# Kernel optimization log

Measured on AMD Instinct MI355X. Metric: run time of the kernel, lower is better.

The kernel has to match this reference:

```python
import jax, jax.numpy as jnp
import numpy as np

HIDDEN = 2048
NUM_HEADS = 16
NUM_KV_HEADS = 4
HEAD_DIM = HIDDEN // NUM_HEADS  # 128
GROUPS = NUM_HEADS // NUM_KV_HEADS  # 4
ROPE_DIMS = 32
QK_GAIN = 6.0
B, T = 2, 2048


def _rope_cos_sin(T, dtype):
    pos = jnp.arange(T, dtype=jnp.float32)
    inv_freq = 1.0 / (10000.0 ** (jnp.arange(0, ROPE_DIMS, 2, dtype=jnp.float32) / ROPE_DIMS))
    freqs = jnp.outer(pos, inv_freq)                  # [T, ROPE/2]
    freqs = jnp.concatenate([freqs, freqs], axis=-1)  # [T, ROPE]
    return jnp.cos(freqs).astype(dtype), jnp.sin(freqs).astype(dtype)


def _apply_rope(t, cos_f, sin_f):
    # t: [B, H, T, head_dim]; rope on first ROPE_DIMS, pass-through on the rest
    t_rt, t_pass = t[..., :ROPE_DIMS], t[..., ROPE_DIMS:]
    h1, h2 = jnp.split(t_rt, 2, axis=-1)
    rot = jnp.concatenate([-h2, h1], axis=-1)
    return jnp.concatenate([t_rt * cos_f + rot * sin_f, t_pass], axis=-1)


def setup_inputs() -> dict:
    key = jax.random.key(0)
    ks = jax.random.split(key, 5)
    s = 0.02
    return {
        "x": jax.random.normal(ks[0], (B, T, HIDDEN), jnp.float32),
        "Wq": jax.random.normal(ks[1], (HIDDEN, HIDDEN), jnp.float32) * s,
        "Wk": jax.random.normal(ks[2], (HIDDEN, NUM_KV_HEADS * HEAD_DIM), jnp.float32) * s,
        "Wv": jax.random.normal(ks[3], (HIDDEN, NUM_KV_HEADS * HEAD_DIM), jnp.float32) * s,
        "Wo": jax.random.normal(ks[4], (HIDDEN, HIDDEN), jnp.float32) * s,
    }


def reference(x, Wq, Wk, Wv, Wo):
    Bx, Tx, C = x.shape
    q = (x @ Wq).reshape(Bx, Tx, NUM_HEADS, HEAD_DIM).transpose(0, 2, 1, 3)      # [B,H,T,d]
    k = (x @ Wk).reshape(Bx, Tx, NUM_KV_HEADS, HEAD_DIM).transpose(0, 2, 1, 3)   # [B,KV,T,d]
    v = (x @ Wv).reshape(Bx, Tx, NUM_KV_HEADS, HEAD_DIM).transpose(0, 2, 1, 3)   # [B,KV,T,d]

    cos_f, sin_f = _rope_cos_sin(Tx, q.dtype)  # [T, ROPE]
    q = _apply_rope(q, cos_f, sin_f)
    k = _apply_rope(k, cos_f, sin_f)

    # GQA: group query heads per kv head instead of repeat_interleave-ing K/V
    qg = q.reshape(Bx, NUM_KV_HEADS, GROUPS, Tx, HEAD_DIM)
    scale = QK_GAIN / jnp.sqrt(jnp.asarray(HEAD_DIM, q.dtype))
    scores = jnp.einsum('bkgqd,bkld->bkgql', qg * scale, k)  # [B,KV,G,T,T]
    causal = jnp.tril(jnp.ones((Tx, Tx), dtype=bool))
    scores = jnp.where(causal, scores, jnp.asarray(-jnp.inf, scores.dtype))
    probs = jax.nn.softmax(scores, axis=-1)
    out = jnp.einsum('bkgql,bkld->bkgqd', probs, v)          # [B,KV,G,T,d]
    out = out.reshape(Bx, NUM_HEADS, Tx, HEAD_DIM).transpose(0, 2, 1, 3).reshape(Bx, Tx, C)
    return out @ Wo
```

## Files before the change

### kernel.cpp

```cpp
#include <hip/hip_runtime.h>
#include <hip/hip_bf16.h>
#include <cstdint>
#include <cstddef>

typedef unsigned short u16;
typedef short s16x8 __attribute__((ext_vector_type(8)));
typedef float f32x4 __attribute__((ext_vector_type(4)));
typedef float f32x16 __attribute__((ext_vector_type(16)));
typedef u16 u16x4 __attribute__((ext_vector_type(4)));

#define HIDDEN_C 2048
#define TSEQ 2048
#define BATCH 2
#define NHEADS 16
#define NKV 4
#define HDIM 128
#define NQKV 3072
#define BTR 4096
#define QK_SCALE 0.53033008588991f

__device__ __forceinline__ float bf2f(u16 u) {
  union { uint32_t i; float f; } v; v.i = ((uint32_t)u) << 16; return v.f;
}
__device__ __forceinline__ u16 f2bf(float f) {
  union { float f; uint32_t i; } v; v.f = f;
  uint32_t r = v.i + 0x7fffu + ((v.i >> 16) & 1u);
  return (u16)(r >> 16);
}

#define AS1(p) ((__attribute__((address_space(1))) void*)(uintptr_t)(p))
#define AS3(p) ((__attribute__((address_space(3))) void*)(p))

__global__ void prep_kernel(const float* __restrict__ x, u16* __restrict__ xb,
                            float2* __restrict__ tab,
                            const float* __restrict__ Wq,
                            const float* __restrict__ Wk,
                            const float* __restrict__ Wv,
                            const float* __restrict__ Wo,
                            u16* __restrict__ wqkvT,
                            u16* __restrict__ woT) {
  const int z = blockIdx.z;
  int tx = threadIdx.x, ty = threadIdx.y;
  if (z == 4) {
    int tid = ty * 32 + tx;
    int bid = blockIdx.y * 64 + blockIdx.x;
    int gi = bid * 256 + tid;
    if (gi < TSEQ * 16) {
      int t = gi >> 4, i = gi & 15;
      float f = powf(10000.f, -(float)i * (1.f / 16.f));
      float ang = (float)t * f;
      tab[gi] = make_float2(cosf(ang), sinf(ang));
    }
    int i = gi * 8;
    float4 a = *(const float4*)(x + i);
    float4 b = *(const float4*)(x + i + 4);
    uint4 o;
    o.x = (uint32_t)f2bf(a.x) | ((uint32_t)f2bf(a.y) << 16);
    o.y = (uint32_t)f2bf(a.z) | ((uint32_t)f2bf(a.w) << 16);
    o.z = (uint32_t)f2bf(b.x) | ((uint32_t)f2bf(b.y) << 16);
    o.w = (uint32_t)f2bf(b.z) | ((uint32_t)f2bf(b.w) << 16);
    *(uint4*)(xb + i) = o;
    return;
  }
  const float* in; u16* out; int C;
  switch (z) {
    case 0: in = Wq; out = wqkvT;                        C = 2048; break;
    case 1: in = Wk; out = wqkvT + (size_t)2048 * 2048;  C = 512;  break;
    case 2: in = Wv; out = wqkvT + (size_t)2560 * 2048;  C = 512;  break;
    default: in = Wo; out = woT;                         C = 2048; break;
  }
  int r0 = blockIdx.y * 32, c0 = blockIdx.x * 32;
  if (c0 >= C) return;
  __shared__ float tile[32][33];
  #pragma unroll
  for (int i = 0; i < 32; i += 8)
    tile[ty + i][tx] = in[(size_t)(r0 + ty + i) * C + c0 + tx];
  __syncthreads();
  #pragma unroll
  for (int i = 0; i < 32; i += 8)
    out[(size_t)(c0 + ty + i) * 2048 + r0 + tx] = f2bf(tile[tx][ty + i]);
}

template <typename OutT>
__global__ __launch_bounds__(256) void gemm_bt_kernel(const u16* __restrict__ A,
                                                      const u16* __restrict__ BT,
                                                      OutT* __restrict__ C,
                                                      int M, int N, int K,
                                                      const float2* __restrict__ tab,
                                                      int mode) {
  __shared__ u16 As[128 * 64];
  __shared__ u16 Bs[128 * 64];
  const int tid = threadIdx.x;
  const int wave = tid >> 6, lane = tid & 63;
  const int lr = lane & 15, lg = lane >> 4;
  const int m0 = blockIdx.y * 128, n0 = blockIdx.x * 128;
  const int wr = wave >> 1, wc = wave & 1;
  const int fsw = (lr & 7) << 3;
  f32x4 acc[4][4];
  #pragma unroll
  for (int a = 0; a < 4; ++a)
    #pragma unroll
    for (int b = 0; b < 4; ++b) acc[a][b] = (f32x4){0.f, 0.f, 0.f, 0.f};

  for (int k0 = 0; k0 < K; k0 += 64) {
    #pragma unroll
    for (int i = 0; i < 4; ++i) {
      int c = tid + i * 256;
      int row = c >> 3, slot = c & 7;
      int gslot = slot ^ (row & 7);
      const u16* gA = A + (size_t)(m0 + row) * K + k0 + gslot * 8;
      const u16* gB = BT + (size_t)(n0 + row) * K + k0 + gslot * 8;
      char* lA = (char*)As + (size_t)c * 16;
      char* lB = (char*)Bs + (size_t)c * 16;
      __builtin_amdgcn_global_load_lds(AS1(gA), AS3(lA), 16, 0, 0);
      __builtin_amdgcn_global_load_lds(AS1(gB), AS3(lB), 16, 0, 0);
    }
    __syncthreads();
    #pragma unroll
    for (int kk = 0; kk < 2; ++kk) {
      s16x8 af[4], bfr[4];
      #pragma unroll
      for (int mi = 0; mi < 4; ++mi)
        af[mi] = *(const s16x8*)(As + (wr * 64 + mi * 16 + lr) * 64 + ((kk * 32 + lg * 8) ^ fsw));
      #pragma unroll
      for (int ni = 0; ni < 4; ++ni)
        bfr[ni] = *(const s16x8*)(Bs + (wc * 64 + ni * 16 + lr) * 64 + ((kk * 32 + lg * 8) ^ fsw));
      #pragma unroll
      for (int mi = 0; mi < 4; ++mi)
        #pragma unroll
        for (int ni = 0; ni < 4; ++ni)
          acc[mi][ni] = __builtin_amdgcn_mfma_f32_16x16x32_bf16(af[mi], bfr[ni], acc[mi][ni], 0, 0, 0);
    }
    __syncthreads();
  }
  if (mode) {
    if (n0 < 2560 && wc == 0) {
      #pragma unroll
      for (int mi = 0; mi < 4; ++mi) {
        int rowb = m0 + wr * 64 + mi * 16 + lg * 4;
        #pragma unroll
        for (int r = 0; r < 4; ++r) {
          int t = (rowb + r) & (TSEQ - 1);
          float2 cs = tab[(t << 4) | lr];
          float a = acc[mi][0][r], b2 = acc[mi][1][r];
          acc[mi][0][r] = a * cs.x - b2 * cs.y;
          acc[mi][1][r] = b2 * cs.x + a * cs.y;
        }
      }
    }
    if (n0 < 2048) {
      #pragma unroll
      for (int mi = 0; mi < 4; ++mi)
        #pragma unroll
        for (int ni = 0; ni < 4; ++ni)
          #pragma unroll
          for (int r = 0; r < 4; ++r) acc[mi][ni][r] *= QK_SCALE;
    }
  }
  #pragma unroll
  for (int mi = 0; mi < 4; ++mi) {
    int rowb = m0 + wr * 64 + mi * 16 + lg * 4;
    #pragma unroll
    for (int ni = 0; ni < 4; ++ni) {
      int col = n0 + wc * 64 + ni * 16 + lr;
      #pragma unroll
      for (int r = 0; r < 4; ++r) {
        float v = acc[mi][ni][r];
        if constexpr (sizeof(OutT) == 2) C[(size_t)(rowb + r) * N + col] = (OutT)f2bf(v);
        else                             C[(size_t)(rowb + r) * N + col] = v;
      }
    }
  }
}

__global__ void transpose_v_kernel(const u16* __restrict__ qkv, u16* __restrict__ vt) {
  int bg = blockIdx.z;
  int b = bg >> 2, g = bg & 3;
  int t0 = blockIdx.x * 32, d0 = blockIdx.y * 32;
  __shared__ u16 tile[32][33];
  int tx = threadIdx.x, ty = threadIdx.y;
  #pragma unroll
  for (int i = 0; i < 32; i += 8)
    tile[ty + i][tx] = qkv[(size_t)(b * TSEQ + t0 + ty + i) * NQKV + 2560 + g * HDIM + d0 + tx];
  __syncthreads();
  #pragma unroll
  for (int i = 0; i < 32; i += 8)
    vt[((size_t)bg * HDIM + d0 + ty + i) * TSEQ + t0 + tx] = tile[tx][ty + i];
}

__global__ __launch_bounds__(256, 2) void attn_kernel(const u16* __restrict__ qkv,
                                                      const u16* __restrict__ vt,
                                                      u16* __restrict__ attn_out) {
  __shared__ u16 K_lds[2][64][128];
  __shared__ u16 V_lds[2][128][64];
  __shared__ u16 P_lds[4][32][64];

  const int idx = blockIdx.x;
  const int h = idx & 15, b = (idx >> 4) & 1, g = h >> 2;
  const int jb = (idx >> 5) & 7;
  const int tile = (idx >> 8) ? jb : 15 - jb;
  const int tid = threadIdx.x, w = tid >> 6, lane = tid & 63;
  const int lq = lane & 31;
  const int hf = lane >> 5;
  const int q0 = tile * 128;
  const int q0w = q0 + w * 32;
  const int kswz = (lq & 15) << 3;
  const int vswz = (lane & 7) << 3;
  const int pswz = lq & 7;

  const u16* Qg = qkv + (size_t)b * TSEQ * NQKV + h * HDIM;
  const u16* Kg = qkv + (size_t)b * TSEQ * NQKV + HIDDEN_C + g * HDIM;
  const u16* Vg = vt + (size_t)(b * NKV + g) * HDIM * TSEQ;

  s16x8 aq[8];
  {
    const u16* qrow = Qg + (size_t)(q0w + lq) * NQKV + hf * 8;
    #pragma unroll
    for (int ds = 0; ds < 8; ++ds) aq[ds] = *(const s16x8*)(qrow + ds * 16);
  }

  f32x16 O[4];
  #pragma unroll
  for (int dt = 0; dt < 4; ++dt)
    #pragma unroll
    for (int r = 0; r < 16; ++r) O[dt][r] = 0.f;
  float m_r = -1e30f, l_r = 0.f;

  auto STAGE = [&](int buf, int kb) {
    #pragma unroll
    for (int i = 0; i < 4; ++i) {
      int c = tid + i * 256;
      int row = c >> 4, slot = c & 15;
      int gslot = slot ^ (row & 15);
      const u16* src = Kg + (size_t)(kb + row) * NQKV + gslot * 8;
      char* dst = (char*)&K_lds[buf][0][0] + (size_t)c * 16;
      __builtin_amdgcn_global_load_lds(AS1(src), AS3(dst), 16, 0, 0);
    }
    #pragma unroll
    for (int i = 0; i < 4; ++i) {
      int c = tid + i * 256;
      int row = c >> 3, slot = c & 7;
      int gslot = slot ^ (row & 7);
      const u16* src = Vg + (size_t)row * TSEQ + kb + gslot * 8;
      char* dst = (char*)&V_lds[buf][0][0] + (size_t)c * 16;
      __builtin_amdgcn_global_load_lds(AS1(src), AS3(dst), 16, 0, 0);
    }
  };

  const int nt = (q0 + 128) / 64;
  STAGE(0, 0);
  asm volatile("s_waitcnt vmcnt(0)" ::: "memory");
  __syncthreads();

  for (int t = 0; t < nt; ++t) {
    const int kb = t * 64;
    const int cur = t & 1;
    if (t + 1 < nt) STAGE(cur ^ 1, kb + 64);

    if (kb <= q0w + 31) {
      f32x16 S[2];
      #pragma unroll
      for (int kh = 0; kh < 2; ++kh)
        #pragma unroll
        for (int r = 0; r < 16; ++r) S[kh][r] = 0.f;
      __builtin_amdgcn_s_setprio(1);
      #pragma unroll
      for (int kh = 0; kh < 2; ++kh) {
        const u16* krow = &K_lds[cur][kh * 32 + lq][0];
        #pragma unroll
        for (int ds = 0; ds < 8; ++ds) {
          s16x8 ak = *(const s16x8*)(krow + ((ds * 16 + hf * 8) ^ kswz));
          S[kh] = __builtin_amdgcn_mfma_f32_32x32x16_bf16(ak, aq[ds], S[kh], 0, 0, 0);
        }
      }
      __builtin_amdgcn_s_setprio(0);
      if (kb + 63 > q0w) {
        const int q = q0w + lq;
        #pragma unroll
        for (int kh = 0; kh < 2; ++kh)
          #pragma unroll
          for (int r = 0; r < 16; ++r) {
            int k = kb + kh * 32 + (r & 3) + 8 * (r >> 2) + 4 * hf;
            if (k > q) S[kh][r] = -1e30f;
          }
      }
      f32x16 pm;
      #pragma unroll
      for (int r = 0; r < 16; ++r) pm[r] = fmaxf(S[0][r], S[1][r]);
      float m8[8];
      #pragma unroll
      for (int r = 0; r < 8; ++r) m8[r] = fmaxf(pm[r], pm[r + 8]);
      float mx = fmaxf(fmaxf(fmaxf(m8[0], m8[4]), fmaxf(m8[1], m8[5])),
                       fmaxf(fmaxf(m8[2], m8[6]), fmaxf(m8[3], m8[7])));
      mx = fmaxf(mx, __shfl_xor(mx, 32));
      if (!__all(mx <= m_r + 8.f)) {
        const float mn = fmaxf(m_r, mx);
        const float al = __expf(m_r - mn);
        m_r = mn;
        l_r *= al;
        #pragma unroll
        for (int dt = 0; dt < 4; ++dt)
          #pragma unroll
          for (int r = 0; r < 16; ++r) O[dt][r] *= al;
      }
      #pragma unroll
      for (int kh = 0; kh < 2; ++kh)
        #pragma unroll
        for (int r = 0; r < 16; ++r) S[kh][r] = __expf(S[kh][r] - m_r);
      f32x16 sv;
      #pragma unroll
      for (int r = 0; r < 16; ++r) sv[r] = S[0][r] + S[1][r];
      float s8[8];
      #pragma unroll
      for (int r = 0; r < 8; ++r) s8[r] = sv[r] + sv[r + 8];
      float ps = ((s8[0] + s8[4]) + (s8[1] + s8[5])) + ((s8[2] + s8[6]) + (s8[3] + s8[7]));
      ps += __shfl_xor(ps, 32);
      l_r += ps;
      u16* pw = &P_lds[w][lq][0];
      #pragma unroll
      for (int kh = 0; kh < 2; ++kh)
        #pragma unroll
        for (int r2 = 0; r2 < 4; ++r2) {
          u16x4 hq;
          #pragma unroll
          for (int j = 0; j < 4; ++j) hq[j] = f2bf(S[kh][r2 * 4 + j]);
          int slot = kh * 4 + r2;
          *(u16x4*)(pw + ((slot ^ pswz) << 3) + hf * 4) = hq;
        }
      asm volatile("s_waitcnt lgkmcnt(0)" ::: "memory");
      __builtin_amdgcn_sched_barrier(0);
      s16x8 pb[4];
      #pragma unroll
      for (int ks = 0; ks < 4; ++ks) {
        int slot = ks * 2 + hf;
        pb[ks] = *(const s16x8*)(pw + ((slot ^ pswz) << 3));
      }
      __builtin_amdgcn_s_setprio(1);
      #pragma unroll
      for (int dt = 0; dt < 4; ++dt) {
        const u16* vrow = &V_lds[cur][dt * 32 + lq][0];
        #pragma unroll
        for (int ks = 0; ks < 4; ++ks) {
          s16x8 av = *(const s16x8*)(vrow + ((ks * 16 + hf * 8) ^ vswz));
          O[dt] = __builtin_amdgcn_mfma_f32_32x32x16_bf16(av, pb[ks], O[dt], 0, 0, 0);
        }
      }
      __builtin_amdgcn_s_setprio(0);
    }
    asm volatile("s_waitcnt vmcnt(0)" ::: "memory");
    __syncthreads();
  }

  const float invl = 1.f / l_r;
  u16* orow = attn_out + (size_t)(b * TSEQ + q0w + lq) * HIDDEN_C + h * HDIM + hf * 4;
  #pragma unroll
  for (int dt = 0; dt < 4; ++dt)
    #pragma unroll
    for (int r2 = 0; r2 < 4; ++r2) {
      u16x4 o4;
      #pragma unroll
      for (int j = 0; j < 4; ++j) o4[j] = f2bf(O[dt][r2 * 4 + j] * invl);
      *(u16x4*)(orow + dt * 32 + r2 * 8) = o4;
    }
}

extern "C" void kernel_launch(void* const* d_in, const int* in_sizes, int n_in,
                              void* d_out, int out_size, void* d_ws, size_t ws_size,
                              hipStream_t stream) {
  const float* x  = (const float*)d_in[0];
  const float* Wq = (const float*)d_in[1];
  const float* Wk = (const float*)d_in[2];
  const float* Wv = (const float*)d_in[3];
  const float* Wo = (const float*)d_in[4];
  float* out = (float*)d_out;
  char* ws = (char*)d_ws;

  u16* xb    = (u16*)(ws);
  u16* wqkvT = (u16*)(ws + (size_t)(16u << 20));
  u16* woT   = (u16*)(ws + (size_t)(28u << 20));
  u16* qkv   = (u16*)(ws + (size_t)(36u << 20));
  u16* vtb   = (u16*)(ws + (size_t)(60u << 20));
  u16* attn  = (u16*)(ws + (size_t)(64u << 20));
  float2* rope_tab = (float2*)(ws + (size_t)(64u << 20));

  dim3 tb(32, 8);
  prep_kernel<<<dim3(64, 64, 5), tb, 0, stream>>>(x, xb, rope_tab, Wq, Wk, Wv, Wo, wqkvT, woT);

  gemm_bt_kernel<u16><<<dim3(NQKV / 128, BTR / 128), 256, 0, stream>>>(
      xb, wqkvT, qkv, BTR, NQKV, HIDDEN_C, rope_tab, 1);

  transpose_v_kernel<<<dim3(TSEQ / 32, HDIM / 32, BATCH * NKV), tb, 0, stream>>>(qkv, vtb);

  attn_kernel<<<512, 256, 0, stream>>>(qkv, vtb, attn);

  gemm_bt_kernel<float><<<dim3(HIDDEN_C / 128, BTR / 128), 256, 0, stream>>>(
      attn, woT, out, BTR, HIDDEN_C, HIDDEN_C, nullptr, 0);
}
```

Measured before the change: 208.8 us.

## Split causal attention KV range into two halves with a separate combine kernel

Each query tile's key range is split in two, doubling the attention grid. Each half writes normalized partial outputs plus per-row max and sum, and a new combine kernel merges them with softmax rescaling. This aims to improve load balance and occupancy across CUs on causal tiles. The cost is an extra kernel launch, extra global traffic for the partial outputs, and a bf16 rounding of intermediate results.

```diff
diff --git a/kernel.cpp b/kernel.cpp
--- a/kernel.cpp
+++ b/kernel.cpp
@@ -190,15 +190,18 @@
 
 __global__ __launch_bounds__(256, 2) void attn_kernel(const u16* __restrict__ qkv,
                                                       const u16* __restrict__ vt,
-                                                      u16* __restrict__ attn_out) {
+                                                      u16* __restrict__ h0out,
+                                                      u16* __restrict__ h1out,
+                                                      float2* __restrict__ ml) {
   __shared__ u16 K_lds[2][64][128];
   __shared__ u16 V_lds[2][128][64];
   __shared__ u16 P_lds[4][32][64];
 
   const int idx = blockIdx.x;
-  const int h = idx & 15, b = (idx >> 4) & 1, g = h >> 2;
-  const int jb = (idx >> 5) & 7;
-  const int tile = (idx >> 8) ? jb : 15 - jb;
+  const int tile = 15 - (idx >> 6);
+  const int half = idx & 1;
+  const int bh = (idx >> 1) & 31;
+  const int h = bh & 15, b = bh >> 4, g = h >> 2;
   const int tid = threadIdx.x, w = tid >> 6, lane = tid & 63;
   const int lq = lane & 31;
   const int hf = lane >> 5;
@@ -247,15 +250,16 @@
     }
   };
 
-  const int nt = (q0 + 128) / 64;
-  STAGE(0, 0);
+  const int t0i = half * (tile + 1);
+  const int t1i = t0i + (tile + 1);
+  STAGE(0, t0i * 64);
   asm volatile("s_waitcnt vmcnt(0)" ::: "memory");
   __syncthreads();
 
-  for (int t = 0; t < nt; ++t) {
-    const int kb = t * 64;
-    const int cur = t & 1;
-    if (t + 1 < nt) STAGE(cur ^ 1, kb + 64);
+  for (int tt = t0i; tt < t1i; ++tt) {
+    const int kb = tt * 64;
+    const int cur = (tt - t0i) & 1;
+    if (tt + 1 < t1i) STAGE(cur ^ 1, kb + 64);
 
     if (kb <= q0w + 31) {
       f32x16 S[2];
@@ -351,8 +355,9 @@
     __syncthreads();
   }
 
-  const float invl = 1.f / l_r;
-  u16* orow = attn_out + (size_t)(b * TSEQ + q0w + lq) * HIDDEN_C + h * HDIM + hf * 4;
+  const float invl = (l_r > 0.f) ? 1.f / l_r : 0.f;
+  u16* obase = (half ? h1out : h0out);
+  u16* orow = obase + (size_t)(b * TSEQ + q0w + lq) * HIDDEN_C + h * HDIM + hf * 4;
   #pragma unroll
   for (int dt = 0; dt < 4; ++dt)
     #pragma unroll
@@ -362,6 +367,38 @@
       for (int j = 0; j < 4; ++j) o4[j] = f2bf(O[dt][r2 * 4 + j] * invl);
       *(u16x4*)(orow + dt * 32 + r2 * 8) = o4;
     }
+  if (hf == 0)
+    ml[(((size_t)half * BATCH + b) * NHEADS + h) * TSEQ + q0w + lq] = make_float2(m_r, l_r);
+}
+
+__global__ void combine_kernel(const u16* __restrict__ h0, u16* __restrict__ h1out,
+                               const float2* __restrict__ ml) {
+  int gi = blockIdx.x * blockDim.x + threadIdx.x;
+  size_t base = (size_t)gi * 8;
+  int bt = (int)(base >> 11);
+  int c = (int)(base & 2047);
+  int h = c >> 7;
+  int b = bt >> 11, q = bt & (TSEQ - 1);
+  float2 v0 = ml[((size_t)(0 * BATCH + b) * NHEADS + h) * TSEQ + q];
+  float2 v1 = ml[((size_t)(1 * BATCH + b) * NHEADS + h) * TSEQ + q];
+  float m = fmaxf(v0.x, v1.x);
+  float w0 = v0.y * __expf(v0.x - m);
+  float w1 = v1.y * __expf(v1.x - m);
+  float inv = 1.f / (w0 + w1);
+  w0 *= inv; w1 *= inv;
+  uint4 a = *(const uint4*)(h0 + base);
+  uint4 d = *(const uint4*)(h1out + base);
+  const uint32_t* au = (const uint32_t*)&a;
+  const uint32_t* du = (const uint32_t*)&d;
+  uint4 o;
+  uint32_t* ou = (uint32_t*)&o;
+  #pragma unroll
+  for (int j = 0; j < 4; ++j) {
+    float lo = bf2f((u16)(au[j] & 0xffff)) * w0 + bf2f((u16)(du[j] & 0xffff)) * w1;
+    float hi = bf2f((u16)(au[j] >> 16)) * w0 + bf2f((u16)(du[j] >> 16)) * w1;
+    ou[j] = (uint32_t)f2bf(lo) | ((uint32_t)f2bf(hi) << 16);
+  }
+  *(uint4*)(h1out + base) = o;
 }
 
 extern "C" void kernel_launch(void* const* d_in, const int* in_sizes, int n_in,
@@ -382,6 +419,7 @@
   u16* vtb   = (u16*)(ws + (size_t)(60u << 20));
   u16* attn  = (u16*)(ws + (size_t)(64u << 20));
   float2* rope_tab = (float2*)(ws + (size_t)(64u << 20));
+  float2* mlbuf = (float2*)(ws + (size_t)(80u << 20));
 
   dim3 tb(32, 8);
   prep_kernel<<<dim3(64, 64, 5), tb, 0, stream>>>(x, xb, rope_tab, Wq, Wk, Wv, Wo, wqkvT, woT);
@@ -391,7 +429,9 @@
 
   transpose_v_kernel<<<dim3(TSEQ / 32, HDIM / 32, BATCH * NKV), tb, 0, stream>>>(qkv, vtb);
 
-  attn_kernel<<<512, 256, 0, stream>>>(qkv, vtb, attn);
+  attn_kernel<<<1024, 256, 0, stream>>>(qkv, vtb, xb, attn, mlbuf);
+
+  combine_kernel<<<(BTR * HIDDEN_C / 8) / 256, 256, 0, stream>>>(xb, attn, mlbuf);
 
   gemm_bt_kernel<float><<<dim3(HIDDEN_C / 128, BTR / 128), 256, 0, stream>>>(
       attn, woT, out, BTR, HIDDEN_C, HIDDEN_C, nullptr, 0);
```

Result: no change. 206.7 us (-1.0%).
